# Performance work log

Hardware: AMD Instinct MI355X
Metric: run time of the kernel (lower is better)

The kernel has to match this reference:

```python
import jax, jax.numpy as jnp
import numpy as np
from jax import lax

BN_EPS = 1e-5

SOBEL_X = np.array([[[[1, 0, -1], [2, 0, -2], [1, 0, -1]]]], dtype=np.float32)
SOBEL_Y = np.array([[[[1, 2, 1], [0, 0, 0], [-1, -2, -1]]]], dtype=np.float32)


def setup_inputs() -> dict:
    key = jax.random.key(0)
    k1, k2, k3 = jax.random.split(key, 3)
    B, C_in, C_out, H, W = 8, 64, 64, 256, 256
    feature_map = jax.random.normal(k1, (B, C_in, H, W), dtype=jnp.float32)
    # kaiming-ish conv init
    conv_w = jax.random.normal(k2, (C_out, C_in, 3, 3), dtype=jnp.float32) * (1.0 / np.sqrt(C_in * 9))
    conv_b = jax.random.normal(k3, (C_out,), dtype=jnp.float32) * 0.01
    bn_gamma = jnp.ones((C_out,), dtype=jnp.float32)
    bn_beta = jnp.zeros((C_out,), dtype=jnp.float32)
    # Learnable filters are initialized (via .data overwrite) to 3x3 Sobel kernels
    filt_x = jnp.asarray(SOBEL_X)
    filt_y = jnp.asarray(SOBEL_Y)
    return {"feature_map": feature_map, "conv_w": conv_w, "conv_b": conv_b,
            "bn_gamma": bn_gamma, "bn_beta": bn_beta, "filt_x": filt_x, "filt_y": filt_y}


def _forward(feature_map, conv_w, conv_b, bn_gamma, bn_beta, filt_x, filt_y):
    # Conv2d(3x3, stride 1, pad 1)
    x = lax.conv_general_dilated(
        feature_map, conv_w, window_strides=(1, 1), padding=((1, 1), (1, 1)),
        dimension_numbers=("NCHW", "OIHW", "NCHW"))
    x = x + conv_b[None, :, None, None]
    # BatchNorm2d (training mode: batch statistics, biased variance)
    mean = jnp.mean(x, axis=(0, 2, 3), keepdims=True)
    var = jnp.mean(jnp.square(x - mean), axis=(0, 2, 3), keepdims=True)
    x = (x - mean) * lax.rsqrt(var + BN_EPS)
    x = x * bn_gamma[None, :, None, None] + bn_beta[None, :, None, None]
    x = jax.nn.relu(x)

    B, C, H, W = x.shape
    # FFT-based circular convolution with zero-padded filters at origin
    Xf = jnp.fft.fft2(x, axes=(-2, -1))  # [B,C,H,W] complex
    pad_h, pad_w = H - filt_x.shape[-2], W - filt_x.shape[-1]
    fx = jnp.pad(filt_x, ((0, 0), (0, 0), (0, pad_h), (0, pad_w)))
    fy = jnp.pad(filt_y, ((0, 0), (0, 0), (0, pad_h), (0, pad_w)))
    Fx = jnp.fft.fft2(fx, axes=(-2, -1))  # [1,1,H,W]
    Fy = jnp.fft.fft2(fy, axes=(-2, -1))

    grad_x = jnp.fft.ifft2(Xf * Fx, axes=(-2, -1)).real
    grad_y = jnp.fft.ifft2(Xf * Fy, axes=(-2, -1)).real

    second_xx = jnp.fft.ifft2(jnp.fft.fft2(grad_x, axes=(-2, -1)) * Fx, axes=(-2, -1)).real
    second_yy = jnp.fft.ifft2(jnp.fft.fft2(grad_y, axes=(-2, -1)) * Fy, axes=(-2, -1)).real

    curvature = (second_xx + second_yy
                 + jnp.square(grad_x) + jnp.square(grad_y)
                 - 2.0 * grad_x * grad_y
                 + x)
    return curvature


def reference(feature_map, conv_w, conv_b, bn_gamma, bn_beta, filt_x, filt_y):
    return _forward(feature_map, conv_w, conv_b, bn_gamma, bn_beta, filt_x, filt_y)
```

## Files before the change

kernel.cpp:

```cpp
#include <hip/hip_runtime.h>

#define BATCH 8
#define HH 256
#define WW 256
#define BN_EPS 1e-5f

#define WS_A 128
#define WS_B 192
#define WS_COEF 256
#define WA_OFF   4096ull
#define PART_OFF 131072ull
#define XT_OFF   4456448ull
#define Y_OFF    73400320ull

typedef __attribute__((ext_vector_type(8))) short bf16x8;
typedef __attribute__((ext_vector_type(4))) float f32x4;

__device__ __forceinline__ unsigned short f2bf(float f) {
    unsigned u = __float_as_uint(f);
    u += 0x7fffu + ((u >> 16) & 1u);
    return (unsigned short)(u >> 16);
}
__device__ __forceinline__ float bf2f(unsigned short s) {
    return __uint_as_float(((unsigned)s) << 16);
}

__global__ __launch_bounds__(256) void transpose_x(const float* __restrict__ in,
                                                   int4* __restrict__ xt) {
    const int row = blockIdx.x, b = blockIdx.y;
    const int tid = threadIdx.x;
    const int cg = tid & 63, kb0 = tid >> 6;
    const int base_in = (b << 22) + (row << 8);
    const int rowblk = (b * 258 + row + 1) * 2064;
    for (int kb = kb0; kb < 8; kb += 4) {
        float v[8][4];
        #pragma unroll
        for (int j = 0; j < 8; ++j) {
            float4 f = *(const float4*)&in[base_in + ((kb * 8 + j) << 16) + cg * 4];
            v[j][0] = f.x; v[j][1] = f.y; v[j][2] = f.z; v[j][3] = f.w;
        }
        #pragma unroll
        for (int cc = 0; cc < 4; ++cc) {
            int col = cg * 4 + cc + 1;
            union { short s[8]; int4 q; } u;
            #pragma unroll
            for (int j = 0; j < 8; ++j) u.s[j] = (short)f2bf(v[j][cc]);
            xt[rowblk + col * 8 + (kb ^ (col & 7))] = u.q;
        }
    }
}

__global__ void pad_xt(int4* __restrict__ xt) {
    int i = blockIdx.x * 256 + threadIdx.x;
    if (i >= 8 * 8224) return;
    int b = i / 8224, r = i - b * 8224;
    int blk;
    if (r < 4128) {
        int row = (r < 2064) ? 0 : 257;
        int off = (r < 2064) ? r : r - 2064;
        blk = (b * 258 + row) * 2064 + off;
    } else {
        int r2 = r - 4128;
        int row = 1 + (r2 >> 4);
        int s = r2 & 15;
        int col = (s < 8) ? 0 : 257;
        blk = (b * 258 + row) * 2064 + col * 8 + (s & 7);
    }
    xt[blk] = make_int4(0, 0, 0, 0);
}

__global__ void transpose_w(const float* __restrict__ wgt, int4* __restrict__ wA) {
    int tid = threadIdx.x;
    for (int e = tid; e < 4608; e += 256) {
        int le = e & 63, f = e >> 6;
        int mt = f & 3, ks = (f >> 2) & 1, t = f >> 3;
        int co = 16 * mt + (le & 15), ci0 = ks * 32 + (le >> 4) * 8;
        union { short s[8]; int4 q; } u;
        #pragma unroll
        for (int j = 0; j < 8; ++j)
            u.s[j] = (short)f2bf(wgt[(co * 64 + ci0 + j) * 9 + t]);
        wA[e] = u.q;
    }
}

__global__ __launch_bounds__(256, 2) void conv_mfma(
        const int4* __restrict__ xt, const int4* __restrict__ wA,
        const float* __restrict__ bias, unsigned short* __restrict__ y,
        float* __restrict__ part) {
    __shared__ int4 xs[6 * 576];
    const int tid = threadIdx.x, lane = tid & 63, wv = tid >> 6;
    const int b = blockIdx.y;
    const int ht = blockIdx.x >> 2, wt = blockIdx.x & 3;
    const int h0 = ht * 4, w0 = wt * 64;
    const int bid = blockIdx.y * 256 + blockIdx.x;

    for (int ch = wv; ch < 54; ch += 4) {
        int row = ch / 9, seg = ch - row * 9;
        xs[row * 576 + seg * 64 + lane] =
            xt[(b * 258 + h0 + row) * 2064 + w0 * 8 + seg * 64 + lane];
    }
    __syncthreads();

    const int q = lane >> 4, n = lane & 15;
    const int r = wv;
    f32x4 acc[4][4] = {};

    #pragma unroll
    for (int t = 0; t < 9; ++t) {
        const int kh = t / 3, kw = t - 3 * (t / 3);
        #pragma unroll
        for (int ks = 0; ks < 2; ++ks) {
            bf16x8 af[4];
            #pragma unroll
            for (int mt = 0; mt < 4; ++mt) {
                int4 v = wA[(8 * t + 4 * ks + mt) * 64 + lane];
                af[mt] = *(bf16x8*)&v;
            }
            bf16x8 bfr[4];
            #pragma unroll
            for (int nt = 0; nt < 4; ++nt) {
                int LC = 16 * nt + n + kw;
                int vq = (ks * 4 + q) ^ (LC & 7);
                bfr[nt] = *(const bf16x8*)&xs[(r + kh) * 576 + LC * 8 + vq];
            }
            #pragma unroll
            for (int mt = 0; mt < 4; ++mt)
                #pragma unroll
                for (int nt = 0; nt < 4; ++nt)
                    acc[mt][nt] = __builtin_amdgcn_mfma_f32_16x16x32_bf16(
                        af[mt], bfr[nt], acc[mt][nt], 0, 0, 0);
        }
    }

    const int gr = h0 + r;
    #pragma unroll
    for (int mt = 0; mt < 4; ++mt) {
        #pragma unroll
        for (int rg = 0; rg < 4; ++rg) {
            int co = 16 * mt + 4 * q + rg;
            float bs = bias[co];
            float s1 = 0.f, s2 = 0.f;
            size_t ybase = ((size_t)(b * 64 + co) << 16) + (gr << 8) + w0 + n;
            #pragma unroll
            for (int nt = 0; nt < 4; ++nt) {
                float yv = acc[mt][nt][rg] + bs;
                y[ybase + 16 * nt] = f2bf(yv);
                s1 += yv; s2 += yv * yv;
            }
            #pragma unroll
            for (int m = 1; m < 16; m <<= 1) {
                s1 += __shfl_xor(s1, m, 64);
                s2 += __shfl_xor(s2, m, 64);
            }
            if (n == 0) {
                part[co * 8192 + bid * 4 + wv] = s1;
                part[64 * 8192 + co * 8192 + bid * 4 + wv] = s2;
            }
        }
    }
}

__global__ void finalize_stats(const float* __restrict__ part,
                               const float* __restrict__ gamma, const float* __restrict__ beta,
                               const float* __restrict__ fx, const float* __restrict__ fy,
                               float* ws) {
    __shared__ float red[512];
    int t = threadIdx.x, co = blockIdx.x;
    if (co < 64) {
        float s1 = 0.f, s2 = 0.f;
        for (int i = t; i < 8192; i += 256) {
            s1 += part[co * 8192 + i];
            s2 += part[64 * 8192 + co * 8192 + i];
        }
        red[t] = s1; red[256 + t] = s2;
        __syncthreads();
        for (int st = 128; st; st >>= 1) {
            if (t < st) { red[t] += red[t + st]; red[256 + t] += red[256 + t + st]; }
            __syncthreads();
        }
        if (t == 0) {
            const float invN = 1.f / 524288.f;
            float m = red[0] * invN;
            float v = red[256] * invN - m * m;
            float a = gamma[co] * rsqrtf(v + BN_EPS);
            ws[WS_A + co] = a;
            ws[WS_B + co] = beta[co] - m * a;
        }
    } else {
        if (t < 25) {
            int c5 = t / 5, d = t % 5;
            float s = 0.f;
            for (int i = 0; i < 3; ++i)
                for (int j = 0; j < 3; ++j) {
                    int i2 = c5 - i, j2 = d - j;
                    if (i2 >= 0 && i2 < 3 && j2 >= 0 && j2 < 3)
                        s += fx[i * 3 + j] * fx[i2 * 3 + j2] + fy[i * 3 + j] * fy[i2 * 3 + j2];
                }
            ws[WS_COEF + t] = s;
        }
        if (t >= 32 && t < 41) ws[WS_COEF + 25 + (t - 32)] = fx[t - 32];
        if (t >= 48 && t < 57) ws[WS_COEF + 34 + (t - 48)] = fy[t - 48];
    }
}

__global__ __launch_bounds__(256) void curvature2(const float* __restrict__ ws,
        const unsigned short* __restrict__ ybuf, float* __restrict__ out) {
    __shared__ float xs[68 * 68];
    __shared__ float cf[43];
    const int tid = threadIdx.x;
    const int c = blockIdx.y, b = blockIdx.z;
    const int h0 = (blockIdx.x >> 2) * 64, w0 = (blockIdx.x & 3) * 64;
    const float a = ws[WS_A + c], bb = ws[WS_B + c];
    const size_t ch = ((size_t)(b * 64 + c)) << 16;
    if (tid < 43) cf[tid] = ws[WS_COEF + tid];
    for (int i = tid; i < 68 * 68; i += 256) {
        int rr = i / 68, cc = i - rr * 68;
        int gh = (h0 - 4 + rr) & 255, gw = (w0 - 4 + cc) & 255;
        float yv = bf2f(ybuf[ch + (gh << 8) + gw]);
        xs[i] = fmaxf(fmaf(yv, a, bb), 0.f);
    }
    __syncthreads();

    const int tx = tid & 15, ty = tid >> 4;
    const int R0 = ty * 4, C0 = tx * 4;
    float p[8][8];
    #pragma unroll
    for (int r8 = 0; r8 < 8; ++r8) {
        float4 u0 = *(float4*)&xs[(R0 + r8) * 68 + C0];
        float4 u1 = *(float4*)&xs[(R0 + r8) * 68 + C0 + 4];
        p[r8][0] = u0.x; p[r8][1] = u0.y; p[r8][2] = u0.z; p[r8][3] = u0.w;
        p[r8][4] = u1.x; p[r8][5] = u1.y; p[r8][6] = u1.z; p[r8][7] = u1.w;
    }
    #pragma unroll
    for (int rr = 0; rr < 4; ++rr) {
        float res[4];
        #pragma unroll
        for (int cc = 0; cc < 4; ++cc) {
            float gx = 0.f, gy = 0.f, kc = 0.f;
            #pragma unroll
            for (int a2 = 0; a2 < 3; ++a2)
                #pragma unroll
                for (int b2 = 0; b2 < 3; ++b2) {
                    float xv = p[rr + 4 - a2][cc + 4 - b2];
                    gx = fmaf(cf[25 + a2 * 3 + b2], xv, gx);
                    gy = fmaf(cf[34 + a2 * 3 + b2], xv, gy);
                }
            #pragma unroll
            for (int c5 = 0; c5 < 5; ++c5)
                #pragma unroll
                for (int d = 0; d < 5; ++d)
                    kc = fmaf(cf[c5 * 5 + d], p[rr + 4 - c5][cc + 4 - d], kc);
            res[cc] = kc + gx * gx + gy * gy - 2.f * gx * gy + p[rr + 4][cc + 4];
        }
        *(float4*)&out[ch + ((size_t)(h0 + R0 + rr) << 8) + w0 + C0] =
            make_float4(res[0], res[1], res[2], res[3]);
    }
}

extern "C" void kernel_launch(void* const* d_in, const int* in_sizes, int n_in,
                              void* d_out, int out_size, void* d_ws, size_t ws_size,
                              hipStream_t stream) {
    const float* in    = (const float*)d_in[0];
    const float* wgt   = (const float*)d_in[1];
    const float* bias  = (const float*)d_in[2];
    const float* gamma = (const float*)d_in[3];
    const float* beta  = (const float*)d_in[4];
    const float* fx    = (const float*)d_in[5];
    const float* fy    = (const float*)d_in[6];
    float* out = (float*)d_out;

    float* wsf = (float*)d_ws;
    int4*  wA   = (int4*)((char*)d_ws + WA_OFF);
    float* part = (float*)((char*)d_ws + PART_OFF);
    int4*  xt   = (int4*)((char*)d_ws + XT_OFF);
    unsigned short* ybuf = (unsigned short*)((char*)d_ws + Y_OFF);

    hipLaunchKernelGGL(transpose_x, dim3(256, 8), dim3(256), 0, stream, in, xt);
    hipLaunchKernelGGL(pad_xt, dim3(257), dim3(256), 0, stream, xt);
    hipLaunchKernelGGL(transpose_w, dim3(1), dim3(256), 0, stream, wgt, wA);
    hipLaunchKernelGGL(conv_mfma, dim3(256, 8), dim3(256), 0, stream,
                       xt, wA, bias, ybuf, part);
    hipLaunchKernelGGL(finalize_stats, dim3(65), dim3(256), 0, stream,
                       part, gamma, beta, fx, fy, wsf);
    hipLaunchKernelGGL(curvature2, dim3(16, 64, 8), dim3(256), 0, stream,
                       wsf, ybuf, out);
}
```

Before: 502.7 us.

## Trim conv LDS tile, vectorize curvature loads, parallelize weight transpose

Spreads the weight transpose across 18 blocks instead of one, shrinks the conv shared tile from 576 to 528 entries per row and raises its occupancy hint to 3 blocks per CU. The curvature kernel now loads bf16 data in 16-byte vectors into a padded 72x84 tile and streams register rows in as they are needed. Its output stores become non-temporal. The aim is less serial preprocessing, higher occupancy and fewer narrow global loads, at the cost of possible register pressure and LDS bank effects from the new strides.

```diff
diff --git a/kernel.cpp b/kernel.cpp
--- a/kernel.cpp
+++ b/kernel.cpp
@@ -70,34 +70,32 @@
 }
 
 __global__ void transpose_w(const float* __restrict__ wgt, int4* __restrict__ wA) {
-    int tid = threadIdx.x;
-    for (int e = tid; e < 4608; e += 256) {
-        int le = e & 63, f = e >> 6;
-        int mt = f & 3, ks = (f >> 2) & 1, t = f >> 3;
-        int co = 16 * mt + (le & 15), ci0 = ks * 32 + (le >> 4) * 8;
-        union { short s[8]; int4 q; } u;
-        #pragma unroll
-        for (int j = 0; j < 8; ++j)
-            u.s[j] = (short)f2bf(wgt[(co * 64 + ci0 + j) * 9 + t]);
-        wA[e] = u.q;
-    }
-}
-
-__global__ __launch_bounds__(256, 2) void conv_mfma(
+    int e = blockIdx.x * 256 + threadIdx.x;
+    if (e >= 4608) return;
+    int le = e & 63, f = e >> 6;
+    int mt = f & 3, ks = (f >> 2) & 1, t = f >> 3;
+    int co = 16 * mt + (le & 15), ci0 = ks * 32 + (le >> 4) * 8;
+    union { short s[8]; int4 q; } u;
+    #pragma unroll
+    for (int j = 0; j < 8; ++j)
+        u.s[j] = (short)f2bf(wgt[(co * 64 + ci0 + j) * 9 + t]);
+    wA[e] = u.q;
+}
+
+__global__ __launch_bounds__(256, 3) void conv_mfma(
         const int4* __restrict__ xt, const int4* __restrict__ wA,
         const float* __restrict__ bias, unsigned short* __restrict__ y,
         float* __restrict__ part) {
-    __shared__ int4 xs[6 * 576];
+    __shared__ int4 xs[6 * 528];
     const int tid = threadIdx.x, lane = tid & 63, wv = tid >> 6;
     const int b = blockIdx.y;
     const int ht = blockIdx.x >> 2, wt = blockIdx.x & 3;
     const int h0 = ht * 4, w0 = wt * 64;
     const int bid = blockIdx.y * 256 + blockIdx.x;
 
-    for (int ch = wv; ch < 54; ch += 4) {
-        int row = ch / 9, seg = ch - row * 9;
-        xs[row * 576 + seg * 64 + lane] =
-            xt[(b * 258 + h0 + row) * 2064 + w0 * 8 + seg * 64 + lane];
+    for (int i = tid; i < 6 * 528; i += 256) {
+        int row = i / 528, j = i - row * 528;
+        xs[i] = xt[(b * 258 + h0 + row) * 2064 + w0 * 8 + j];
     }
     __syncthreads();
 
@@ -121,7 +119,7 @@
             for (int nt = 0; nt < 4; ++nt) {
                 int LC = 16 * nt + n + kw;
                 int vq = (ks * 4 + q) ^ (LC & 7);
-                bfr[nt] = *(const bf16x8*)&xs[(r + kh) * 576 + LC * 8 + vq];
+                bfr[nt] = *(const bf16x8*)&xs[(r + kh) * 528 + LC * 8 + vq];
             }
             #pragma unroll
             for (int mt = 0; mt < 4; ++mt)
@@ -203,9 +201,9 @@
     }
 }
 
-__global__ __launch_bounds__(256) void curvature2(const float* __restrict__ ws,
+__global__ __launch_bounds__(256, 4) void curvature2(const float* __restrict__ ws,
         const unsigned short* __restrict__ ybuf, float* __restrict__ out) {
-    __shared__ float xs[68 * 68];
+    __shared__ float xs[72 * 84];
     __shared__ float cf[43];
     const int tid = threadIdx.x;
     const int c = blockIdx.y, b = blockIdx.z;
@@ -213,11 +211,18 @@
     const float a = ws[WS_A + c], bb = ws[WS_B + c];
     const size_t ch = ((size_t)(b * 64 + c)) << 16;
     if (tid < 43) cf[tid] = ws[WS_COEF + tid];
-    for (int i = tid; i < 68 * 68; i += 256) {
-        int rr = i / 68, cc = i - rr * 68;
-        int gh = (h0 - 4 + rr) & 255, gw = (w0 - 4 + cc) & 255;
-        float yv = bf2f(ybuf[ch + (gh << 8) + gw]);
-        xs[i] = fmaxf(fmaf(yv, a, bb), 0.f);
+
+    for (int i = tid; i < 720; i += 256) {
+        int rr = i / 10, g = i - rr * 10;
+        int gh = (h0 - 4 + rr) & 255;
+        int gw = (w0 - 8 + g * 8) & 255;
+        int4 v = *(const int4*)&ybuf[ch + (gh << 8) + gw];
+        const unsigned short* s = (const unsigned short*)&v;
+        float o[8];
+        #pragma unroll
+        for (int j = 0; j < 8; ++j) o[j] = fmaxf(fmaf(bf2f(s[j]), a, bb), 0.f);
+        *(float4*)&xs[rr * 84 + g * 8]     = make_float4(o[0], o[1], o[2], o[3]);
+        *(float4*)&xs[rr * 84 + g * 8 + 4] = make_float4(o[4], o[5], o[6], o[7]);
     }
     __syncthreads();
 
@@ -225,14 +230,20 @@
     const int R0 = ty * 4, C0 = tx * 4;
     float p[8][8];
     #pragma unroll
-    for (int r8 = 0; r8 < 8; ++r8) {
-        float4 u0 = *(float4*)&xs[(R0 + r8) * 68 + C0];
-        float4 u1 = *(float4*)&xs[(R0 + r8) * 68 + C0 + 4];
-        p[r8][0] = u0.x; p[r8][1] = u0.y; p[r8][2] = u0.z; p[r8][3] = u0.w;
-        p[r8][4] = u1.x; p[r8][5] = u1.y; p[r8][6] = u1.z; p[r8][7] = u1.w;
+    for (int j = 0; j < 5; ++j) {
+        float4 u0 = *(float4*)&xs[(R0 + j) * 84 + C0 + 4];
+        float4 u1 = *(float4*)&xs[(R0 + j) * 84 + C0 + 8];
+        p[j][0] = u0.x; p[j][1] = u0.y; p[j][2] = u0.z; p[j][3] = u0.w;
+        p[j][4] = u1.x; p[j][5] = u1.y; p[j][6] = u1.z; p[j][7] = u1.w;
     }
     #pragma unroll
     for (int rr = 0; rr < 4; ++rr) {
+        if (rr) {
+            float4 u0 = *(float4*)&xs[(R0 + rr + 4) * 84 + C0 + 4];
+            float4 u1 = *(float4*)&xs[(R0 + rr + 4) * 84 + C0 + 8];
+            p[rr + 4][0] = u0.x; p[rr + 4][1] = u0.y; p[rr + 4][2] = u0.z; p[rr + 4][3] = u0.w;
+            p[rr + 4][4] = u1.x; p[rr + 4][5] = u1.y; p[rr + 4][6] = u1.z; p[rr + 4][7] = u1.w;
+        }
         float res[4];
         #pragma unroll
         for (int cc = 0; cc < 4; ++cc) {
@@ -252,8 +263,9 @@
                     kc = fmaf(cf[c5 * 5 + d], p[rr + 4 - c5][cc + 4 - d], kc);
             res[cc] = kc + gx * gx + gy * gy - 2.f * gx * gy + p[rr + 4][cc + 4];
         }
-        *(float4*)&out[ch + ((size_t)(h0 + R0 + rr) << 8) + w0 + C0] =
-            make_float4(res[0], res[1], res[2], res[3]);
+        f32x4 rv = { res[0], res[1], res[2], res[3] };
+        __builtin_nontemporal_store(rv,
+            (f32x4*)&out[ch + ((size_t)(h0 + R0 + rr) << 8) + w0 + C0]);
     }
 }
 
@@ -277,7 +289,7 @@
 
     hipLaunchKernelGGL(transpose_x, dim3(256, 8), dim3(256), 0, stream, in, xt);
     hipLaunchKernelGGL(pad_xt, dim3(257), dim3(256), 0, stream, xt);
-    hipLaunchKernelGGL(transpose_w, dim3(1), dim3(256), 0, stream, wgt, wA);
+    hipLaunchKernelGGL(transpose_w, dim3(18), dim3(256), 0, stream, wgt, wA);
     hipLaunchKernelGGL(conv_mfma, dim3(256, 8), dim3(256), 0, stream,
                        xt, wA, bias, ybuf, part);
     hipLaunchKernelGGL(finalize_stats, dim3(65), dim3(256), 0, stream,
```

Result: slower. 633.8 us (+26.1%).
